# Kernel optimization log

Hardware: AMD Instinct MI355X
Metric: run time of the kernel (lower is better)

Reference implementation:

```python
import jax, jax.numpy as jnp
import numpy as np
import math

A = 256            # n_agents == batch rows (epymarl stacks agents along batch)
B = A
OBS = 512          # obs_shape = (input_shape - n_actions) // 2
NA = 64            # n_actions
MSG = 2048         # messages_shape (divisible by A)
H = 1024           # hidden_dim
T = 3              # trajectory_length
TAU = OBS + NA
VD = MSG // A      # per-agent message dim


def setup_inputs() -> dict:
    key = jax.random.key(0)
    keys = iter(jax.random.split(key, 40))
    def lin(o, i):
        w = jax.random.normal(next(keys), (o, i), jnp.float32) * (i ** -0.5)
        return w, jnp.zeros((o,), jnp.float32)
    d = {}
    d["inputs"] = jax.random.normal(next(keys), (B, 2 * OBS + NA + MSG), jnp.float32)
    d["hidden_state"] = jax.random.normal(next(keys), (B, 3 * H), jnp.float32) * 0.1
    for name, o, i in [("pi_fc1", H, OBS + MSG), ("pi_fc2", NA, H),
                       ("fa_fc1", H, OBS), ("fa_fc2", (A - 1) * NA, H),
                       ("fo_fc1", H, NA * A + OBS), ("fo_fc2", OBS, H),
                       ("am_qs", H, MSG), ("am_ks", H, TAU), ("am_vs", VD, TAU)]:
        d[name + "_w"], d[name + "_b"] = lin(o, i)
    for name in ["pi_rnn", "fa_rnn", "fo_rnn"]:
        d[name + "_wih"], d[name + "_bih"] = lin(3 * H, H)
        d[name + "_whh"], d[name + "_bhh"] = lin(3 * H, H)
    return d


def _gru(x, h, wih, whh, bih, bhh):
    gi = x @ wih.T + bih
    gh = h @ whh.T + bhh
    ir, iz, i_n = jnp.split(gi, 3, -1)
    hr, hz, h_n = jnp.split(gh, 3, -1)
    r = jax.nn.sigmoid(ir + hr)
    z = jax.nn.sigmoid(iz + hz)
    n = jnp.tanh(i_n + r * h_n)
    return (1.0 - z) * n + z * h


def reference(inputs, hidden_state,
              pi_fc1_w, pi_fc1_b, pi_fc2_w, pi_fc2_b,
              pi_rnn_wih, pi_rnn_whh, pi_rnn_bih, pi_rnn_bhh,
              fa_fc1_w, fa_fc1_b, fa_fc2_w, fa_fc2_b,
              fa_rnn_wih, fa_rnn_whh, fa_rnn_bih, fa_rnn_bhh,
              fo_fc1_w, fo_fc1_b, fo_fc2_w, fo_fc2_b,
              fo_rnn_wih, fo_rnn_whh, fo_rnn_bih, fo_rnn_bhh,
              am_qs_w, am_qs_b, am_ks_w, am_ks_b, am_vs_w, am_vs_b):
    sg = jax.lax.stop_gradient
    lin = lambda x, w, b: x @ w.T + b
    h_fa = hidden_state[:, :H]
    h_fo = hidden_state[:, H:2 * H]
    h_pi0 = hidden_state[:, -H:]
    obs = inputs[:, :OBS]
    prev_obs = inputs[:, OBS:2 * OBS]
    prev_act = sg(inputs[:, 2 * OBS:2 * OBS + NA])   # .detach() in torch
    prev_msg = inputs[:, -MSG:]

    def pi(o, m, h):
        x = jax.nn.relu(lin(jnp.concatenate([o, m], -1), pi_fc1_w, pi_fc1_b))
        h2 = _gru(x, h, pi_rnn_wih, pi_rnn_whh, pi_rnn_bih, pi_rnn_bhh)
        return lin(h2, pi_fc2_w, pi_fc2_b), h2

    # ---- ImaginedTrajectory rollout (fixed small T, python loop is structural) ----
    o, a, h_pi = prev_obs, prev_act, h_pi0
    observations, actions = [o], [a]
    for _ in range(T - 1):
        x = jax.nn.relu(lin(o, fa_fc1_w, fa_fc1_b))
        h_fa = _gru(x, h_fa, fa_rnn_wih, fa_rnn_whh, fa_rnn_bih, fa_rnn_bhh)
        q = lin(h_fa, fa_fc2_w, fa_fc2_b)                       # [B,(A-1)*NA]
        qs = jax.nn.softmax(q.reshape(B, A - 1, NA), -1)
        # torch stack(qs_out).reshape(orig): scrambles (A-1,B) order, kept faithfully
        fa = jnp.transpose(qs, (1, 0, 2)).reshape(B, (A - 1) * NA)
        x2 = jax.nn.relu(lin(jnp.concatenate([fa, a, o], -1), fo_fc1_w, fo_fc1_b))
        h_fo = _gru(x2, h_fo, fo_rnn_wih, fo_rnn_whh, fo_rnn_bih, fo_rnn_bhh)
        nxt_o = lin(h_fo, fo_fc2_w, fo_fc2_b)
        nxt_a, h_pi = pi(sg(o), sg(prev_msg), sg(h_pi))         # forward_pi detaches inputs
        o, a = nxt_o, nxt_a
        observations.append(o)
        actions.append(a)
    taus = jnp.stack([jnp.concatenate([observations[t], actions[t]], -1)
                      for t in range(T)])                        # [T,B,TAU]

    # ---- AttentionMechanism: batched equivalent of the per-agent python loops ----
    # k rows are indexed j*n_agents + i with batch == n_agents, i.e. k[t, b] here.
    qv = lin(prev_msg, am_qs_w, am_qs_b)                         # [B,H]
    kk = jnp.einsum('tbi,hi->tbh', taus, am_ks_w) + am_ks_b      # [T,B,H]
    vv = jnp.einsum('tbi,vi->tbv', taus, am_vs_w) + am_vs_b      # [T,B,VD]
    alpha = jax.nn.softmax(jnp.einsum('bh,tbh->bt', qv, kk) / math.sqrt(H), -1)
    new_message = jnp.einsum('bt,tbv->bv', alpha, vv)            # [B,VD]

    # cat([msg]*A, 0).reshape(B,-1): each agent receives all agents' messages
    pi_msg = jnp.tile(new_message, (A, 1)).reshape(B, -1)        # [B,MSG]
    action, h_pi_f = pi(obs, pi_msg, h_pi0)                      # uses ORIGINAL h_pi slice
    h_out = jnp.concatenate([h_fa, h_fo, h_pi_f], -1)            # [B,3H]
    q_out = jnp.concatenate([new_message, action], -1)           # [B,VD+NA]
    return q_out, h_out
```

## Files before the change

kernel.cpp:

```cpp
#include <hip/hip_runtime.h>
#include <hip/hip_bf16.h>
#include <math.h>

#define OBS 512
#define MSG 2048
#define TAU 576
#define TAUP 640
#define QN 16320
#define X2W 16896
#define INW 3136
#define PIW 2560

typedef short short8v __attribute__((ext_vector_type(8)));
typedef float f32x4 __attribute__((ext_vector_type(4)));
typedef __hip_bfloat16 bf;

__device__ inline unsigned short bfbits(float x) {
  bf h = __float2bfloat16(x);
  return *reinterpret_cast<unsigned short*>(&h);
}

__device__ inline ushort4 cvtf4(float4 v) {
  ushort4 r;
  r.x = bfbits(v.x); r.y = bfbits(v.y); r.z = bfbits(v.z); r.w = bfbits(v.w);
  return r;
}

__device__ inline void gload16(const void* g, void* l) {
  __builtin_amdgcn_global_load_lds((__attribute__((address_space(1))) void*)(g),
                                   (__attribute__((address_space(3))) void*)(l), 16, 0, 0);
}

struct MMSet {
  const bf* A;
  const float* W;
  const float* bias;
  float* C;
  bf* Cb;
  int lda, ldw, ldc, ldcb;
};

template<int ACT, bool ATOMIC, bool DUAL>
__global__ __launch_bounds__(256)
void k_mm(MMSet s0, MMSet s1, int kSteps)
{
  __shared__ bf As[2][64 * 64];
  __shared__ bf Bs[2][64 * 64];
  const MMSet S = (DUAL && blockIdx.z) ? s1 : s0;
  const int tid = threadIdx.x;
  const int lane = tid & 63;
  const int wid = tid >> 6;
  const int m0 = blockIdx.y * 64;
  const int n0 = blockIdx.x * 64;
  const size_t k0 = ATOMIC ? (size_t)blockIdx.z * kSteps * 64 : 0;

  const bf* Ab = S.A + (size_t)m0 * S.lda + k0;
  const float* Bb = S.W + (size_t)n0 * S.ldw + k0;

  int arow[2], acol[2], adst[2];
#pragma unroll
  for (int r = 0; r < 2; ++r) {
    int chunk = r * 256 + tid;
    arow[r] = chunk >> 3;
    acol[r] = ((chunk & 7) ^ (arow[r] & 7)) * 8;
    adst[r] = chunk * 8;
  }
  int brow[4], bcol[4], bdst[4];
#pragma unroll
  for (int r = 0; r < 4; ++r) {
    int c = r * 256 + tid;
    brow[r] = c >> 4;
    int g = (c & 15) >> 1, half = c & 1;
    bcol[r] = (c & 15) * 4;
    bdst[r] = brow[r] * 64 + ((g ^ (brow[r] & 7)) << 3) + half * 4;
  }

  const int wr = wid >> 1, wc = wid & 1;
  const int fr = lane & 15, q = lane >> 4;
  const int xm = fr & 7;

  f32x4 acc00 = {}, acc01 = {}, acc10 = {}, acc11 = {};
  float4 w0, w1, w2, w3;

  auto stageA = [&](int buf, int kt) {
#pragma unroll
    for (int r = 0; r < 2; ++r)
      gload16(Ab + (size_t)arow[r] * S.lda + kt + acol[r], &As[buf][adst[r]]);
  };
  auto loadB = [&](int kt) {
    w0 = *(const float4*)(Bb + (size_t)brow[0] * S.ldw + kt + bcol[0]);
    w1 = *(const float4*)(Bb + (size_t)brow[1] * S.ldw + kt + bcol[1]);
    w2 = *(const float4*)(Bb + (size_t)brow[2] * S.ldw + kt + bcol[2]);
    w3 = *(const float4*)(Bb + (size_t)brow[3] * S.ldw + kt + bcol[3]);
  };
  auto writeB = [&](int buf) {
    *(ushort4*)&Bs[buf][bdst[0]] = cvtf4(w0);
    *(ushort4*)&Bs[buf][bdst[1]] = cvtf4(w1);
    *(ushort4*)&Bs[buf][bdst[2]] = cvtf4(w2);
    *(ushort4*)&Bs[buf][bdst[3]] = cvtf4(w3);
  };

  stageA(0, 0);
  loadB(0);
  writeB(0);
  __syncthreads();

  for (int t = 0; t < kSteps; ++t) {
    const int buf = t & 1;
    if (t + 1 < kSteps) {
      stageA(buf ^ 1, (t + 1) * 64);
      loadB((t + 1) * 64);
    }
    const bf* Ac = As[buf];
    const bf* Bc = Bs[buf];
#pragma unroll
    for (int ks = 0; ks < 2; ++ks) {
      const int cc = ks * 4 + q;
      const int co = ((cc ^ xm) << 3);
      short8v a0 = *(const short8v*)&Ac[(wr * 32 +  0 + fr) * 64 + co];
      short8v a1 = *(const short8v*)&Ac[(wr * 32 + 16 + fr) * 64 + co];
      short8v b0 = *(const short8v*)&Bc[(wc * 32 +  0 + fr) * 64 + co];
      short8v b1 = *(const short8v*)&Bc[(wc * 32 + 16 + fr) * 64 + co];
      acc00 = __builtin_amdgcn_mfma_f32_16x16x32_bf16(a0, b0, acc00, 0, 0, 0);
      acc01 = __builtin_amdgcn_mfma_f32_16x16x32_bf16(a0, b1, acc01, 0, 0, 0);
      acc10 = __builtin_amdgcn_mfma_f32_16x16x32_bf16(a1, b0, acc10, 0, 0, 0);
      acc11 = __builtin_amdgcn_mfma_f32_16x16x32_bf16(a1, b1, acc11, 0, 0, 0);
    }
    if (t + 1 < kSteps) writeB(buf ^ 1);
    __syncthreads();
  }

  const int mb0 = m0 + wr * 32 + q * 4;
  const int mb1 = mb0 + 16;
  const int nc0 = n0 + wc * 32 + fr;
  const int nc1 = nc0 + 16;
  if (ATOMIC) {
#pragma unroll
    for (int v = 0; v < 4; ++v) {
      atomicAdd(&S.C[(size_t)(mb0 + v) * S.ldc + nc0], acc00[v]);
      atomicAdd(&S.C[(size_t)(mb0 + v) * S.ldc + nc1], acc01[v]);
      atomicAdd(&S.C[(size_t)(mb1 + v) * S.ldc + nc0], acc10[v]);
      atomicAdd(&S.C[(size_t)(mb1 + v) * S.ldc + nc1], acc11[v]);
    }
  } else {
    const float bb0 = S.bias[nc0], bb1 = S.bias[nc1];
#pragma unroll
    for (int v = 0; v < 4; ++v) {
      float v00 = acc00[v] + bb0, v01 = acc01[v] + bb1;
      float v10 = acc10[v] + bb0, v11 = acc11[v] + bb1;
      if (ACT) { v00 = fmaxf(v00, 0.f); v01 = fmaxf(v01, 0.f);
                 v10 = fmaxf(v10, 0.f); v11 = fmaxf(v11, 0.f); }
      if (S.C) {
        S.C[(size_t)(mb0 + v) * S.ldc + nc0] = v00;
        S.C[(size_t)(mb0 + v) * S.ldc + nc1] = v01;
        S.C[(size_t)(mb1 + v) * S.ldc + nc0] = v10;
        S.C[(size_t)(mb1 + v) * S.ldc + nc1] = v11;
      }
      if (S.Cb) {
        S.Cb[(size_t)(mb0 + v) * S.ldcb + nc0] = __float2bfloat16(v00);
        S.Cb[(size_t)(mb0 + v) * S.ldcb + nc1] = __float2bfloat16(v01);
        S.Cb[(size_t)(mb1 + v) * S.ldcb + nc0] = __float2bfloat16(v10);
        S.Cb[(size_t)(mb1 + v) * S.ldcb + nc1] = __float2bfloat16(v11);
      }
    }
  }
}

__global__ __launch_bounds__(256)
void k_init(const float* __restrict__ in, const float* __restrict__ hid,
            float* __restrict__ h32a, float* __restrict__ h32o, float* __restrict__ h32p,
            bf* __restrict__ hba, bf* __restrict__ hbo,
            bf* __restrict__ hbp, bf* __restrict__ hbp0,
            bf* __restrict__ taus, bf* __restrict__ msgb,
            const float* __restrict__ fo1b, float* __restrict__ xf0, float* __restrict__ xf1,
            const float* __restrict__ pi1b, float* __restrict__ xp0,
            float* __restrict__ xp1, float* __restrict__ xp2)
{
  const int bx = blockIdx.x;
  if (bx < 3072) {
    int idx = bx * 256 + threadIdx.x;
    int b = idx / 3072, c = idx % 3072;
    float v = hid[idx];
    bf hb = __float2bfloat16(v);
    int j = c & 1023;
    if (c < 1024)      { h32a[b * 1024 + j] = v; hba[b * 1024 + j] = hb; }
    else if (c < 2048) { h32o[b * 1024 + j] = v; hbo[b * 1024 + j] = hb; }
    else               { h32p[b * 1024 + j] = v; hbp[b * 1024 + j] = hb; hbp0[b * 1024 + j] = hb; }
  } else if (bx < 3072 + 1920) {
    int idx = (bx - 3072) * 256 + threadIdx.x;
    int t = idx / (256 * TAUP);
    int r = (idx / TAUP) % 256;
    int c = idx % TAUP;
    float v = 0.f;
    if (t == 0 && c < TAU)
      v = (c < OBS) ? in[(size_t)r * INW + OBS + c]
                    : in[(size_t)r * INW + 2 * OBS + (c - OBS)];
    taus[idx] = __float2bfloat16(v);
  } else if (bx < 3072 + 1920 + 2048) {
    int idx = (bx - 3072 - 1920) * 256 + threadIdx.x;
    int b = idx >> 11, c = idx & 2047;
    msgb[idx] = __float2bfloat16(in[(size_t)b * INW + 1088 + c]);
  } else if (bx < 3072 + 1920 + 2048 + 1024) {
    int idx = (bx - 3072 - 1920 - 2048) * 256 + threadIdx.x;
    float v = fo1b[idx & 1023];
    xf0[idx] = v; xf1[idx] = v;
  } else {
    int idx = (bx - 3072 - 1920 - 2048 - 1024) * 256 + threadIdx.x;
    float v = pi1b[idx & 1023];
    xp0[idx] = v; xp1[idx] = v; xp2[idx] = v;
  }
}

__global__ __launch_bounds__(256)
void k_gru(const float* __restrict__ gi, const float* __restrict__ gh,
           const float* __restrict__ hs, int ldsrc,
           float* __restrict__ hd, int lddst, bf* __restrict__ hb)
{
  int idx = blockIdx.x * 256 + threadIdx.x;
  int b = idx >> 10, j = idx & 1023;
  float ir = gi[b * 3072 + j];
  float iz = gi[b * 3072 + 1024 + j];
  float in_ = gi[b * 3072 + 2048 + j];
  float hr = gh[b * 3072 + j];
  float hz = gh[b * 3072 + 1024 + j];
  float hn = gh[b * 3072 + 2048 + j];
  float r = 1.f / (1.f + expf(-(ir + hr)));
  float z = 1.f / (1.f + expf(-(iz + hz)));
  float n = tanhf(in_ + r * hn);
  float h = hs[(size_t)b * ldsrc + j];
  float o = (1.f - z) * n + z * h;
  hd[(size_t)b * lddst + j] = o;
  hb[idx] = __float2bfloat16(o);
}

__global__ __launch_bounds__(256)
void k_softmax_scatter(const bf* __restrict__ q, bf* __restrict__ x2)
{
  int wid = blockIdx.x * 4 + (threadIdx.x >> 6);
  int lane = threadIdx.x & 63;
  int b = wid / 255, p = wid % 255;
  float v = __bfloat162float(q[(size_t)b * QN + p * 64 + lane]);
  float m = v;
#pragma unroll
  for (int s = 32; s; s >>= 1) m = fmaxf(m, __shfl_xor(m, s));
  float e = expf(v - m);
  float sum = e;
#pragma unroll
  for (int s = 32; s; s >>= 1) sum += __shfl_xor(sum, s);
  float r = e / sum;
  int flat = p * 16384 + b * 64 + lane;
  int bp = flat / QN;
  int j = flat - bp * QN;
  x2[(size_t)bp * X2W + j] = __float2bfloat16(r);
}

__global__ __launch_bounds__(256)
void k_x2_tail(const bf* __restrict__ taus_t, bf* __restrict__ x2)
{
  int idx = blockIdx.x * 256 + threadIdx.x;
  int b = idx / TAU, c = idx % TAU;
  if (c < 64)
    x2[(size_t)b * X2W + QN + c] = taus_t[(size_t)b * TAUP + OBS + c];
  else
    x2[(size_t)b * X2W + QN + 64 + (c - 64)] = taus_t[(size_t)b * TAUP + (c - 64)];
}

__global__ __launch_bounds__(256)
void k_concat_pi_loop(const bf* __restrict__ taus_t, const bf* __restrict__ msg,
                      bf* __restrict__ piin)
{
  int idx = blockIdx.x * 256 + threadIdx.x;
  int b = idx / PIW, c = idx % PIW;
  piin[idx] = (c < OBS) ? taus_t[(size_t)b * TAUP + c] : msg[b * MSG + (c - OBS)];
}

__global__ __launch_bounds__(256)
void k_concat_pi_final(const float* __restrict__ in, const float* __restrict__ nm,
                       bf* __restrict__ piin)
{
  int idx = blockIdx.x * 256 + threadIdx.x;
  int b = idx / PIW, c = idx % PIW;
  float v = (c < OBS) ? in[(size_t)b * INW + c] : nm[c - OBS];
  piin[idx] = __float2bfloat16(v);
}

__global__ __launch_bounds__(256)
void k_relu_cvt(const float* __restrict__ s, bf* __restrict__ d)
{
  int idx = blockIdx.x * 256 + threadIdx.x;
  d[idx] = __float2bfloat16(fmaxf(s[idx], 0.f));
}

__global__ __launch_bounds__(64)
void k_vv(const bf* __restrict__ taus, const float* __restrict__ w,
          const float* __restrict__ bias, float* __restrict__ vv)
{
  int row = blockIdx.x;
  int lane = threadIdx.x;
  const bf* tr = taus + (size_t)row * TAUP;
  for (int v = 0; v < 8; ++v) {
    float s = 0.f;
    for (int k = lane; k < TAU; k += 64) s += __bfloat162float(tr[k]) * w[v * TAU + k];
#pragma unroll
    for (int d = 32; d; d >>= 1) s += __shfl_xor(s, d);
    if (lane == 0) vv[row * 8 + v] = s + bias[v];
  }
}

__global__ __launch_bounds__(64)
void k_attn(const float* __restrict__ qv, const float* __restrict__ kk,
            const float* __restrict__ vv, float* __restrict__ nm,
            float* __restrict__ out_q)
{
  int b = blockIdx.x;
  int lane = threadIdx.x;
  const float* qb = qv + (size_t)b * 1024;
  float s[3];
#pragma unroll
  for (int t = 0; t < 3; ++t) {
    const float* kb = kk + (size_t)(t * 256 + b) * 1024;
    float acc = 0.f;
    for (int h = lane; h < 1024; h += 64) acc += qb[h] * kb[h];
#pragma unroll
    for (int d = 32; d; d >>= 1) acc += __shfl_xor(acc, d);
    s[t] = acc * (1.f / 32.f);
  }
  float m = fmaxf(s[0], fmaxf(s[1], s[2]));
  float e0 = expf(s[0] - m), e1 = expf(s[1] - m), e2 = expf(s[2] - m);
  float inv = 1.f / (e0 + e1 + e2);
  float a0 = e0 * inv, a1 = e1 * inv, a2 = e2 * inv;
  if (lane < 8) {
    float v = a0 * vv[(0 * 256 + b) * 8 + lane]
            + a1 * vv[(1 * 256 + b) * 8 + lane]
            + a2 * vv[(2 * 256 + b) * 8 + lane];
    nm[b * 8 + lane] = v;
    out_q[b * 72 + lane] = v;
  }
}

__global__ __launch_bounds__(256)
void k_copy_hout(const float* __restrict__ hfa, const float* __restrict__ hfo,
                 float* __restrict__ hout)
{
  int idx = blockIdx.x * 256 + threadIdx.x;
  int b = idx / 2048, c = idx % 2048;
  float v = (c < 1024) ? hfa[b * 1024 + c] : hfo[b * 1024 + (c - 1024)];
  hout[(size_t)b * 3072 + c] = v;
}

extern "C" void kernel_launch(void* const* d_in, const int* in_sizes, int n_in,
                              void* d_out_v, int out_size, void* d_ws, size_t ws_size,
                              hipStream_t stream)
{
  const float* inputs   = (const float*)d_in[0];
  const float* hidden   = (const float*)d_in[1];
  const float* pi_fc1_w = (const float*)d_in[2];
  const float* pi_fc1_b = (const float*)d_in[3];
  const float* pi_fc2_w = (const float*)d_in[4];
  const float* pi_fc2_b = (const float*)d_in[5];
  const float* fa_fc1_w = (const float*)d_in[6];
  const float* fa_fc1_b = (const float*)d_in[7];
  const float* fa_fc2_w = (const float*)d_in[8];
  const float* fa_fc2_b = (const float*)d_in[9];
  const float* fo_fc1_w = (const float*)d_in[10];
  const float* fo_fc1_b = (const float*)d_in[11];
  const float* fo_fc2_w = (const float*)d_in[12];
  const float* fo_fc2_b = (const float*)d_in[13];
  const float* am_qs_w  = (const float*)d_in[14];
  const float* am_qs_b  = (const float*)d_in[15];
  const float* am_ks_w  = (const float*)d_in[16];
  const float* am_ks_b  = (const float*)d_in[17];
  const float* am_vs_w  = (const float*)d_in[18];
  const float* am_vs_b  = (const float*)d_in[19];
  const float* pi_wih   = (const float*)d_in[20];
  const float* pi_bih   = (const float*)d_in[21];
  const float* pi_whh   = (const float*)d_in[22];
  const float* pi_bhh   = (const float*)d_in[23];
  const float* fa_wih   = (const float*)d_in[24];
  const float* fa_bih   = (const float*)d_in[25];
  const float* fa_whh   = (const float*)d_in[26];
  const float* fa_bhh   = (const float*)d_in[27];
  const float* fo_wih   = (const float*)d_in[28];
  const float* fo_bih   = (const float*)d_in[29];
  const float* fo_whh   = (const float*)d_in[30];
  const float* fo_bhh   = (const float*)d_in[31];

  float* out = (float*)d_out_v;
  char* p = (char*)d_ws;
  auto alloc = [&](size_t bytes) { void* r = p; p += (bytes + 255) & ~(size_t)255; return r; };

  bf* HFAB = (bf*)alloc((size_t)256 * 1024 * 2);
  bf* HFOB = (bf*)alloc((size_t)256 * 1024 * 2);
  bf* HPIB = (bf*)alloc((size_t)256 * 1024 * 2);
  bf* HPI0B = (bf*)alloc((size_t)256 * 1024 * 2);
  bf* XBUFB = (bf*)alloc((size_t)256 * 1024 * 2);
  bf* TAUSB = (bf*)alloc((size_t)3 * 256 * TAUP * 2);
  bf* X2B  = (bf*)alloc((size_t)256 * X2W * 2);
  bf* PIINB = (bf*)alloc((size_t)256 * PIW * 2);
  bf* MSGB = (bf*)alloc((size_t)256 * MSG * 2);
  bf* QBUFB = (bf*)alloc((size_t)256 * QN * 2);
  float* HFA32 = (float*)alloc((size_t)256 * 1024 * 4);
  float* HFO32 = (float*)alloc((size_t)256 * 1024 * 4);
  float* HPI32 = (float*)alloc((size_t)256 * 1024 * 4);
  float* XF32A = (float*)alloc((size_t)256 * 1024 * 4);
  float* XF32B = (float*)alloc((size_t)256 * 1024 * 4);
  float* XP32A = (float*)alloc((size_t)256 * 1024 * 4);
  float* XP32B = (float*)alloc((size_t)256 * 1024 * 4);
  float* XP32C = (float*)alloc((size_t)256 * 1024 * 4);
  float* GI = (float*)alloc((size_t)256 * 3072 * 4);
  float* GH = (float*)alloc((size_t)256 * 3072 * 4);
  float* QV = (float*)alloc((size_t)256 * 1024 * 4);
  float* KK = (float*)alloc((size_t)768 * 1024 * 4);
  float* VV = (float*)alloc((size_t)768 * 8 * 4);
  float* NM = (float*)alloc((size_t)2048 * 4);

  auto mset = [&](const bf* A, int lda, const float* W, int ldw, const float* bias,
                  float* C, int ldc, bf* Cb, int ldcb) {
    MMSet s; s.A = A; s.W = W; s.bias = bias; s.C = C; s.Cb = Cb;
    s.lda = lda; s.ldw = ldw; s.ldc = ldc; s.ldcb = ldcb; return s;
  };
  auto mm = [&](MMSet a, int M, int N, int K, int act) {
    dim3 g(N / 64, M / 64, 1);
    if (act) k_mm<1, false, false><<<g, 256, 0, stream>>>(a, a, K / 64);
    else     k_mm<0, false, false><<<g, 256, 0, stream>>>(a, a, K / 64);
  };
  auto mmAtomic = [&](const bf* A, int lda, const float* W, int ldw,
                      float* C, int M, int N, int K, int z) {
    MMSet s = mset(A, lda, W, ldw, nullptr, C, N, nullptr, 0);
    dim3 g(N / 64, M / 64, z);
    k_mm<0, true, false><<<g, 256, 0, stream>>>(s, s, K / (64 * z));
  };
  auto mmDual = [&](MMSet a, MMSet b, int N, int K) {
    dim3 g(N / 64, 4, 2);
    k_mm<0, false, true><<<g, 256, 0, stream>>>(a, b, K / 64);
  };

  k_init<<<3072 + 1920 + 2048 + 1024 + 1024, 256, 0, stream>>>(inputs, hidden,
      HFA32, HFO32, HPI32, HFAB, HFOB, HPIB, HPI0B, TAUSB, MSGB,
      fo_fc1_b, XF32A, XF32B, pi_fc1_b, XP32A, XP32B, XP32C);

  for (int t = 0; t < 2; ++t) {
    bf* taus_t = TAUSB + (size_t)t * 256 * TAUP;
    bf* taus_n = TAUSB + (size_t)(t + 1) * 256 * TAUP;
    float* xf32 = t ? XF32B : XF32A;
    float* xp32 = t ? XP32B : XP32A;
    mm(mset(taus_t, TAUP, fa_fc1_w, 512, fa_fc1_b, nullptr, 0, XBUFB, 1024), 256, 1024, 512, 1);
    mmDual(mset(XBUFB, 1024, fa_wih, 1024, fa_bih, GI, 3072, nullptr, 0),
           mset(HFAB, 1024, fa_whh, 1024, fa_bhh, GH, 3072, nullptr, 0), 3072, 1024);
    k_gru<<<1024, 256, 0, stream>>>(GI, GH, HFA32, 1024, HFA32, 1024, HFAB);
    mm(mset(HFAB, 1024, fa_fc2_w, 1024, fa_fc2_b, nullptr, 0, QBUFB, QN), 256, QN, 1024, 0);
    k_x2_tail<<<576, 256, 0, stream>>>(taus_t, X2B);
    k_softmax_scatter<<<16320, 256, 0, stream>>>(QBUFB, X2B);
    mmAtomic(X2B, X2W, fo_fc1_w, X2W, xf32, 256, 1024, X2W, 12);
    k_relu_cvt<<<1024, 256, 0, stream>>>(xf32, XBUFB);
    mmDual(mset(XBUFB, 1024, fo_wih, 1024, fo_bih, GI, 3072, nullptr, 0),
           mset(HFOB, 1024, fo_whh, 1024, fo_bhh, GH, 3072, nullptr, 0), 3072, 1024);
    k_gru<<<1024, 256, 0, stream>>>(GI, GH, HFO32, 1024, HFO32, 1024, HFOB);
    mm(mset(HFOB, 1024, fo_fc2_w, 1024, fo_fc2_b, nullptr, 0, taus_n, TAUP), 256, 512, 1024, 0);
    k_concat_pi_loop<<<2560, 256, 0, stream>>>(taus_t, MSGB, PIINB);
    mmAtomic(PIINB, PIW, pi_fc1_w, PIW, xp32, 256, 1024, PIW, 4);
    k_relu_cvt<<<1024, 256, 0, stream>>>(xp32, XBUFB);
    mmDual(mset(XBUFB, 1024, pi_wih, 1024, pi_bih, GI, 3072, nullptr, 0),
           mset(HPIB, 1024, pi_whh, 1024, pi_bhh, GH, 3072, nullptr, 0), 3072, 1024);
    k_gru<<<1024, 256, 0, stream>>>(GI, GH, HPI32, 1024, HPI32, 1024, HPIB);
    mm(mset(HPIB, 1024, pi_fc2_w, 1024, pi_fc2_b, nullptr, 0, taus_n + OBS, TAUP), 256, 64, 1024, 0);
  }

  mm(mset(MSGB, MSG, am_qs_w, MSG, am_qs_b, QV, 1024, nullptr, 0), 256, 1024, 2048, 0);
  mm(mset(TAUSB, TAUP, am_ks_w, TAU, am_ks_b, KK, 1024, nullptr, 0), 768, 1024, TAU, 0);
  k_vv<<<768, 64, 0, stream>>>(TAUSB, am_vs_w, am_vs_b, VV);
  k_attn<<<256, 64, 0, stream>>>(QV, KK, VV, NM, out);

  k_concat_pi_final<<<2560, 256, 0, stream>>>(inputs, NM, PIINB);
  mmAtomic(PIINB, PIW, pi_fc1_w, PIW, XP32C, 256, 1024, PIW, 4);
  k_relu_cvt<<<1024, 256, 0, stream>>>(XP32C, XBUFB);
  mmDual(mset(XBUFB, 1024, pi_wih, 1024, pi_bih, GI, 3072, nullptr, 0),
         mset(HPI0B, 1024, pi_whh, 1024, pi_bhh, GH, 3072, nullptr, 0), 3072, 1024);
  k_gru<<<1024, 256, 0, stream>>>(GI, GH, hidden + 2048, 3072,
                                  out + 256 * 72 + 2048, 3072, HPIB);
  mm(mset(HPIB, 1024, pi_fc2_w, 1024, pi_fc2_b, out + 8, 72, nullptr, 0), 256, 64, 1024, 0);
  k_copy_hout<<<2048, 256, 0, stream>>>(HFA32, HFO32, out + 256 * 72);
  (void)in_sizes; (void)n_in; (void)out_size; (void)ws_size;
}
```

Measured before the change: 637.0 us.

## Replace shared GEMM with weight-streaming per-wave kernel and merge small launches

The 64x64 block-tiled bf16 GEMM is replaced by a 512-thread kernel. Each of its 8 waves owns 32 rows of M, keeps A fragments in registers loaded straight from global memory, and streams fp32 weight tiles into a private LDS double buffer with global_load_lds, waiting on vmcnt and using no block barriers. All M=256 rows now share one pass over the weights, so the mostly weight-bound GEMMs read each weight once instead of once per 64-row tile. The fo_fc2 and pi_fc2 GEMMs are merged into one launch. The am_qs projection moves to the start as a split-K atomic GEMM, with its bias preloaded in k_init. The fo_fc1 split-K factor changes from 12 to 11. Risks are fewer blocks per launch, less parallelism, and fragile hand-written waitcnt scheduling.

Result: slower. 782.8 us (+22.9%).

```diff
diff --git a/kernel.cpp b/kernel.cpp
--- a/kernel.cpp
+++ b/kernel.cpp
@@ -26,9 +26,24 @@
   return r;
 }
 
+__device__ inline short8v pack8(ushort4 u0, ushort4 u1) {
+  union { short8v v; ushort4 u[2]; } t;
+  t.u[0] = u0; t.u[1] = u1;
+  return t.v;
+}
+
 __device__ inline void gload16(const void* g, void* l) {
   __builtin_amdgcn_global_load_lds((__attribute__((address_space(1))) void*)(g),
                                    (__attribute__((address_space(3))) void*)(l), 16, 0, 0);
+}
+
+__device__ inline void wait_vm6() {
+  asm volatile("s_waitcnt vmcnt(6)" ::: "memory");
+  __builtin_amdgcn_sched_barrier(0);
+}
+__device__ inline void wait_vm0() {
+  asm volatile("s_waitcnt vmcnt(0)" ::: "memory");
+  __builtin_amdgcn_sched_barrier(0);
 }
 
 struct MMSet {
@@ -40,99 +55,89 @@
   int lda, ldw, ldc, ldcb;
 };
 
-template<int ACT, bool ATOMIC, bool DUAL>
-__global__ __launch_bounds__(256)
-void k_mm(MMSet s0, MMSet s1, int kSteps)
-{
-  __shared__ bf As[2][64 * 64];
-  __shared__ bf Bs[2][64 * 64];
-  const MMSet S = (DUAL && blockIdx.z) ? s1 : s0;
-  const int tid = threadIdx.x;
-  const int lane = tid & 63;
-  const int wid = tid >> 6;
-  const int m0 = blockIdx.y * 64;
-  const int n0 = blockIdx.x * 64;
-  const size_t k0 = ATOMIC ? (size_t)blockIdx.z * kSteps * 64 : 0;
-
-  const bf* Ab = S.A + (size_t)m0 * S.lda + k0;
-  const float* Bb = S.W + (size_t)n0 * S.ldw + k0;
-
-  int arow[2], acol[2], adst[2];
-#pragma unroll
-  for (int r = 0; r < 2; ++r) {
-    int chunk = r * 256 + tid;
-    arow[r] = chunk >> 3;
-    acol[r] = ((chunk & 7) ^ (arow[r] & 7)) * 8;
-    adst[r] = chunk * 8;
-  }
-  int brow[4], bcol[4], bdst[4];
-#pragma unroll
-  for (int r = 0; r < 4; ++r) {
-    int c = r * 256 + tid;
-    brow[r] = c >> 4;
-    int g = (c & 15) >> 1, half = c & 1;
-    bcol[r] = (c & 15) * 4;
-    bdst[r] = brow[r] * 64 + ((g ^ (brow[r] & 7)) << 3) + half * 4;
-  }
-
-  const int wr = wid >> 1, wc = wid & 1;
+template<int ACT, bool ATOMIC, bool DUAL, bool DUALX>
+__global__ __launch_bounds__(512)
+void k_wp(MMSet s0, MMSet s1, int kSteps, int nsplit)
+{
+  __shared__ float Bs[8][2][1024];
+  const int bx = blockIdx.x;
+  const MMSet S = DUALX ? (bx < nsplit ? s0 : s1)
+                        : ((DUAL && blockIdx.z) ? s1 : s0);
+  const int nblk = DUALX ? (bx < nsplit ? bx : bx - nsplit) : bx;
+  const int tid = threadIdx.x, lane = tid & 63, wid = tid >> 6;
   const int fr = lane & 15, q = lane >> 4;
-  const int xm = fr & 7;
+  const int m0 = (blockIdx.y * 8 + wid) * 32;
+  const int n0 = nblk * 32;
+  const size_t k0 = (ATOMIC) ? (size_t)blockIdx.z * kSteps * 32 : 0;
+
+  const float* bsrc[4];
+#pragma unroll
+  for (int i = 0; i < 4; ++i) {
+    int idx = i * 64 + lane, row = idx >> 3, c = idx & 7;
+    bsrc[i] = S.W + (size_t)(n0 + row) * S.ldw + k0 + ((c ^ (row & 7)) * 4);
+  }
+  float* myB0 = &Bs[wid][0][0];
+  float* myB1 = &Bs[wid][1][0];
+
+  const bf* Ap0 = S.A + (size_t)(m0 + fr) * S.lda + k0 + q * 8;
+  const bf* Ap1 = Ap0 + (size_t)16 * S.lda;
 
   f32x4 acc00 = {}, acc01 = {}, acc10 = {}, acc11 = {};
-  float4 w0, w1, w2, w3;
-
-  auto stageA = [&](int buf, int kt) {
-#pragma unroll
-    for (int r = 0; r < 2; ++r)
-      gload16(Ab + (size_t)arow[r] * S.lda + kt + acol[r], &As[buf][adst[r]]);
-  };
-  auto loadB = [&](int kt) {
-    w0 = *(const float4*)(Bb + (size_t)brow[0] * S.ldw + kt + bcol[0]);
-    w1 = *(const float4*)(Bb + (size_t)brow[1] * S.ldw + kt + bcol[1]);
-    w2 = *(const float4*)(Bb + (size_t)brow[2] * S.ldw + kt + bcol[2]);
-    w3 = *(const float4*)(Bb + (size_t)brow[3] * S.ldw + kt + bcol[3]);
-  };
-  auto writeB = [&](int buf) {
-    *(ushort4*)&Bs[buf][bdst[0]] = cvtf4(w0);
-    *(ushort4*)&Bs[buf][bdst[1]] = cvtf4(w1);
-    *(ushort4*)&Bs[buf][bdst[2]] = cvtf4(w2);
-    *(ushort4*)&Bs[buf][bdst[3]] = cvtf4(w3);
-  };
-
-  stageA(0, 0);
-  loadB(0);
-  writeB(0);
-  __syncthreads();
-
-  for (int t = 0; t < kSteps; ++t) {
-    const int buf = t & 1;
-    if (t + 1 < kSteps) {
-      stageA(buf ^ 1, (t + 1) * 64);
-      loadB((t + 1) * 64);
+  short8v a0_0, a1_0, a0_1, a1_1;
+
+  auto issueB = [&](float* buf, int t) {
+    const size_t kt = (size_t)t * 32;
+#pragma unroll
+    for (int i = 0; i < 4; ++i)
+      gload16(bsrc[i] + kt, buf + i * 256);
+  };
+  auto bfrag = [&](const float* buf, int row) {
+    const float* r = buf + row * 32;
+    float4 f0 = *(const float4*)(r + (((2 * q    ) ^ (row & 7)) * 4));
+    float4 f1 = *(const float4*)(r + (((2 * q + 1) ^ (row & 7)) * 4));
+    return pack8(cvtf4(f0), cvtf4(f1));
+  };
+  auto dostep = [&](const float* buf, short8v a0, short8v a1) {
+    short8v b0 = bfrag(buf, fr);
+    short8v b1 = bfrag(buf, fr + 16);
+    acc00 = __builtin_amdgcn_mfma_f32_16x16x32_bf16(a0, b0, acc00, 0, 0, 0);
+    acc01 = __builtin_amdgcn_mfma_f32_16x16x32_bf16(a0, b1, acc01, 0, 0, 0);
+    acc10 = __builtin_amdgcn_mfma_f32_16x16x32_bf16(a1, b0, acc10, 0, 0, 0);
+    acc11 = __builtin_amdgcn_mfma_f32_16x16x32_bf16(a1, b1, acc11, 0, 0, 0);
+  };
+
+  issueB(myB0, 0);
+  a0_0 = *(const short8v*)(Ap0); a1_0 = *(const short8v*)(Ap1);
+  __builtin_amdgcn_sched_barrier(0);
+  issueB(myB1, 1);
+  a0_1 = *(const short8v*)(Ap0 + 32); a1_1 = *(const short8v*)(Ap1 + 32);
+  __builtin_amdgcn_sched_barrier(0);
+
+  for (int t = 0; t < kSteps; t += 2) {
+    wait_vm6();
+    dostep(myB0, a0_0, a1_0);
+    __builtin_amdgcn_sched_barrier(0);
+    const bool more2 = (t + 2 < kSteps);
+    if (more2) {
+      issueB(myB0, t + 2);
+      a0_0 = *(const short8v*)(Ap0 + (t + 2) * 32);
+      a1_0 = *(const short8v*)(Ap1 + (t + 2) * 32);
     }
-    const bf* Ac = As[buf];
-    const bf* Bc = Bs[buf];
-#pragma unroll
-    for (int ks = 0; ks < 2; ++ks) {
-      const int cc = ks * 4 + q;
-      const int co = ((cc ^ xm) << 3);
-      short8v a0 = *(const short8v*)&Ac[(wr * 32 +  0 + fr) * 64 + co];
-      short8v a1 = *(const short8v*)&Ac[(wr * 32 + 16 + fr) * 64 + co];
-      short8v b0 = *(const short8v*)&Bc[(wc * 32 +  0 + fr) * 64 + co];
-      short8v b1 = *(const short8v*)&Bc[(wc * 32 + 16 + fr) * 64 + co];
-      acc00 = __builtin_amdgcn_mfma_f32_16x16x32_bf16(a0, b0, acc00, 0, 0, 0);
-      acc01 = __builtin_amdgcn_mfma_f32_16x16x32_bf16(a0, b1, acc01, 0, 0, 0);
-      acc10 = __builtin_amdgcn_mfma_f32_16x16x32_bf16(a1, b0, acc10, 0, 0, 0);
-      acc11 = __builtin_amdgcn_mfma_f32_16x16x32_bf16(a1, b1, acc11, 0, 0, 0);
+    __builtin_amdgcn_sched_barrier(0);
+    if (more2) wait_vm6(); else wait_vm0();
+    dostep(myB1, a0_1, a1_1);
+    __builtin_amdgcn_sched_barrier(0);
+    if (t + 3 < kSteps) {
+      issueB(myB1, t + 3);
+      a0_1 = *(const short8v*)(Ap0 + (t + 3) * 32);
+      a1_1 = *(const short8v*)(Ap1 + (t + 3) * 32);
     }
-    if (t + 1 < kSteps) writeB(buf ^ 1);
-    __syncthreads();
-  }
-
-  const int mb0 = m0 + wr * 32 + q * 4;
+    __builtin_amdgcn_sched_barrier(0);
+  }
+
+  const int mb0 = m0 + q * 4;
   const int mb1 = mb0 + 16;
-  const int nc0 = n0 + wc * 32 + fr;
+  const int nc0 = n0 + fr;
   const int nc1 = nc0 + 16;
   if (ATOMIC) {
 #pragma unroll
@@ -174,7 +179,8 @@
             bf* __restrict__ taus, bf* __restrict__ msgb,
             const float* __restrict__ fo1b, float* __restrict__ xf0, float* __restrict__ xf1,
             const float* __restrict__ pi1b, float* __restrict__ xp0,
-            float* __restrict__ xp1, float* __restrict__ xp2)
+            float* __restrict__ xp1, float* __restrict__ xp2,
+            const float* __restrict__ qsb, float* __restrict__ qv)
 {
   const int bx = blockIdx.x;
   if (bx < 3072) {
@@ -204,10 +210,13 @@
     int idx = (bx - 3072 - 1920 - 2048) * 256 + threadIdx.x;
     float v = fo1b[idx & 1023];
     xf0[idx] = v; xf1[idx] = v;
-  } else {
+  } else if (bx < 3072 + 1920 + 2048 + 2048) {
     int idx = (bx - 3072 - 1920 - 2048 - 1024) * 256 + threadIdx.x;
     float v = pi1b[idx & 1023];
     xp0[idx] = v; xp1[idx] = v; xp2[idx] = v;
+  } else {
+    int idx = (bx - 3072 - 1920 - 2048 - 2048) * 256 + threadIdx.x;
+    qv[idx] = qsb[idx & 1023];
   }
 }
 
@@ -420,24 +429,30 @@
     s.lda = lda; s.ldw = ldw; s.ldc = ldc; s.ldcb = ldcb; return s;
   };
   auto mm = [&](MMSet a, int M, int N, int K, int act) {
-    dim3 g(N / 64, M / 64, 1);
-    if (act) k_mm<1, false, false><<<g, 256, 0, stream>>>(a, a, K / 64);
-    else     k_mm<0, false, false><<<g, 256, 0, stream>>>(a, a, K / 64);
+    dim3 g(N / 32, M / 256, 1);
+    if (act) k_wp<1, false, false, false><<<g, 512, 0, stream>>>(a, a, K / 32, 0);
+    else     k_wp<0, false, false, false><<<g, 512, 0, stream>>>(a, a, K / 32, 0);
   };
   auto mmAtomic = [&](const bf* A, int lda, const float* W, int ldw,
-                      float* C, int M, int N, int K, int z) {
+                      float* C, int N, int K, int z) {
     MMSet s = mset(A, lda, W, ldw, nullptr, C, N, nullptr, 0);
-    dim3 g(N / 64, M / 64, z);
-    k_mm<0, true, false><<<g, 256, 0, stream>>>(s, s, K / (64 * z));
+    dim3 g(N / 32, 1, z);
+    k_wp<0, true, false, false><<<g, 512, 0, stream>>>(s, s, K / (32 * z), 0);
   };
   auto mmDual = [&](MMSet a, MMSet b, int N, int K) {
-    dim3 g(N / 64, 4, 2);
-    k_mm<0, false, true><<<g, 256, 0, stream>>>(a, b, K / 64);
-  };
-
-  k_init<<<3072 + 1920 + 2048 + 1024 + 1024, 256, 0, stream>>>(inputs, hidden,
+    dim3 g(N / 32, 1, 2);
+    k_wp<0, false, true, false><<<g, 512, 0, stream>>>(a, b, K / 32, 0);
+  };
+  auto mmDualX = [&](MMSet a, int Na, MMSet b, int Nb, int K) {
+    dim3 g((Na + Nb) / 32, 1, 1);
+    k_wp<0, false, false, true><<<g, 512, 0, stream>>>(a, b, K / 32, Na / 32);
+  };
+
+  k_init<<<3072 + 1920 + 2048 + 1024 + 1024 + 1024, 256, 0, stream>>>(inputs, hidden,
       HFA32, HFO32, HPI32, HFAB, HFOB, HPIB, HPI0B, TAUSB, MSGB,
-      fo_fc1_b, XF32A, XF32B, pi_fc1_b, XP32A, XP32B, XP32C);
+      fo_fc1_b, XF32A, XF32B, pi_fc1_b, XP32A, XP32B, XP32C, am_qs_b, QV);
+
+  mmAtomic(MSGB, MSG, am_qs_w, MSG, QV, 1024, 2048, 2);
 
   for (int t = 0; t < 2; ++t) {
     bf* taus_t = TAUSB + (size_t)t * 256 * TAUP;
@@ -451,28 +466,28 @@
     mm(mset(HFAB, 1024, fa_fc2_w, 1024, fa_fc2_b, nullptr, 0, QBUFB, QN), 256, QN, 1024, 0);
     k_x2_tail<<<576, 256, 0, stream>>>(taus_t, X2B);
     k_softmax_scatter<<<16320, 256, 0, stream>>>(QBUFB, X2B);
-    mmAtomic(X2B, X2W, fo_fc1_w, X2W, xf32, 256, 1024, X2W, 12);
+    mmAtomic(X2B, X2W, fo_fc1_w, X2W, xf32, 1024, X2W, 11);
     k_relu_cvt<<<1024, 256, 0, stream>>>(xf32, XBUFB);
     mmDual(mset(XBUFB, 1024, fo_wih, 1024, fo_bih, GI, 3072, nullptr, 0),
            mset(HFOB, 1024, fo_whh, 1024, fo_bhh, GH, 3072, nullptr, 0), 3072, 1024);
     k_gru<<<1024, 256, 0, stream>>>(GI, GH, HFO32, 1024, HFO32, 1024, HFOB);
-    mm(mset(HFOB, 1024, fo_fc2_w, 1024, fo_fc2_b, nullptr, 0, taus_n, TAUP), 256, 512, 1024, 0);
     k_concat_pi_loop<<<2560, 256, 0, stream>>>(taus_t, MSGB, PIINB);
-    mmAtomic(PIINB, PIW, pi_fc1_w, PIW, xp32, 256, 1024, PIW, 4);
+    mmAtomic(PIINB, PIW, pi_fc1_w, PIW, xp32, 1024, PIW, 4);
     k_relu_cvt<<<1024, 256, 0, stream>>>(xp32, XBUFB);
     mmDual(mset(XBUFB, 1024, pi_wih, 1024, pi_bih, GI, 3072, nullptr, 0),
            mset(HPIB, 1024, pi_whh, 1024, pi_bhh, GH, 3072, nullptr, 0), 3072, 1024);
     k_gru<<<1024, 256, 0, stream>>>(GI, GH, HPI32, 1024, HPI32, 1024, HPIB);
-    mm(mset(HPIB, 1024, pi_fc2_w, 1024, pi_fc2_b, nullptr, 0, taus_n + OBS, TAUP), 256, 64, 1024, 0);
-  }
-
-  mm(mset(MSGB, MSG, am_qs_w, MSG, am_qs_b, QV, 1024, nullptr, 0), 256, 1024, 2048, 0);
-  mm(mset(TAUSB, TAUP, am_ks_w, TAU, am_ks_b, KK, 1024, nullptr, 0), 768, 1024, TAU, 0);
+    mmDualX(mset(HFOB, 1024, fo_fc2_w, 1024, fo_fc2_b, nullptr, 0, taus_n, TAUP), 512,
+            mset(HPIB, 1024, pi_fc2_w, 1024, pi_fc2_b, nullptr, 0, taus_n + OBS, TAUP), 64,
+            1024);
+  }
+
+  mm(mset(TAUSB, TAUP, am_ks_w, TAU, am_ks_b, KK, 1024, nullptr, 0), 768, 1024, 576, 0);
   k_vv<<<768, 64, 0, stream>>>(TAUSB, am_vs_w, am_vs_b, VV);
   k_attn<<<256, 64, 0, stream>>>(QV, KK, VV, NM, out);
 
   k_concat_pi_final<<<2560, 256, 0, stream>>>(inputs, NM, PIINB);
-  mmAtomic(PIINB, PIW, pi_fc1_w, PIW, XP32C, 256, 1024, PIW, 4);
+  mmAtomic(PIINB, PIW, pi_fc1_w, PIW, XP32C, 1024, PIW, 4);
   k_relu_cvt<<<1024, 256, 0, stream>>>(XP32C, XBUFB);
   mmDual(mset(XBUFB, 1024, pi_wih, 1024, pi_bih, GI, 3072, nullptr, 0),
          mset(HPI0B, 1024, pi_whh, 1024, pi_bhh, GH, 3072, nullptr, 0), 3072, 1024);
```
